# Kernel tuning notes

Hardware: AMD Instinct MI355X
Metric: run time of the kernel (lower is better)

The kernel has to match this reference:

```python
import jax, jax.numpy as jnp
import numpy as np

N_IN, N_OUT, K, G = 128, 256, 3, 3  # G = grid intervals (setup hard-codes 3)
KNOT_LO, KNOT_HI = -1.0, 1.0


def make_grid(n, k, G, lo=KNOT_LO, hi=KNOT_HI):
    # Augmented knot vector: G+1 knots extended by k on each side -> G+2k+1 points
    h = (hi - lo) / G
    g = jnp.arange(-k, G + k + 1, dtype=jnp.float32) * h + lo
    return jnp.tile(g[None, :], (n, 1))  # (n, G+2k+1)


def get_spline_basis(x, grid, k):
    # Cox-de Boor recursion. x: (batch, n); grid: (n, G+2k+1)
    g = grid[None, :, :]          # (1, n, G+2k+1)
    xx = x[:, :, None]            # (batch, n, 1)
    # order-0 (indicator) basis: (batch, n, G+2k)
    basis = ((xx >= g[..., :-1]) & (xx < g[..., 1:])).astype(x.dtype)
    for kk in range(1, k + 1):
        left = (xx - g[..., : -(kk + 1)]) / (g[..., kk:-1] - g[..., : -(kk + 1)]) * basis[..., :-1]
        right = (g[..., kk + 1 :] - xx) / (g[..., kk + 1 :] - g[..., 1:-kk]) * basis[..., 1:]
        basis = left + right
    return basis  # (batch, n, G+k)


def setup_inputs() -> dict:
    key = jax.random.key(0)
    k1, k2 = jax.random.split(key)
    batch = 512
    n = N_IN * N_OUT
    x = jax.random.normal(k1, (batch, N_IN), dtype=jnp.float32)
    grid = make_grid(n, K, G)                                        # state (non-trainable)
    c_basis = 0.1 * jax.random.normal(k2, (n, G + K), dtype=jnp.float32)
    c_spl = jnp.ones((n,), dtype=jnp.float32)
    c_res = jnp.ones((n,), dtype=jnp.float32)
    return {"x": x, "grid": grid, "c_basis": c_basis, "c_spl": c_spl, "c_res": c_res}


def reference(x, grid, c_basis, c_spl, c_res):
    batch = x.shape[0]
    # Broadcast each input node to every output edge, out-major ordering:
    # einsum('ij,k->ikj', x, ones(n_out)).reshape(batch, n_in*n_out)
    x_ext = jnp.broadcast_to(x[:, None, :], (batch, N_OUT, N_IN)).reshape(batch, N_OUT * N_IN)
    # residual branch: swish, transposed to (n, batch)
    res = jax.nn.swish(x_ext).T
    # spline branch: (batch, n, G+K) basis combined with per-edge coeffs -> (n, batch)
    Bi = get_spline_basis(x_ext, grid, K)
    spl = jnp.einsum('ij,bij->ib', c_basis, Bi)
    y = c_spl[:, None] * spl + c_res[:, None] * res            # (n, batch)
    y = y.reshape(N_OUT, N_IN, batch).sum(axis=1) / N_IN       # (n_out, batch)
    return y.T                                                 # (batch, n_out)
```

## Files before the change

kernel.cpp:

```cpp
#include <hip/hip_runtime.h>
#include <hip/hip_bf16.h>


typedef short short8 __attribute__((ext_vector_type(8)));
typedef float f32x4 __attribute__((ext_vector_type(4)));

static __device__ inline unsigned short bf16_bits(float f) {
    union { __hip_bfloat16 h; unsigned short u; } cvt;
    cvt.h = __float2bfloat16(f);
    return cvt.u;
}

__global__ __launch_bounds__(256) void build_fw(
    const float* __restrict__ x,
    const float* __restrict__ grid,
    const float* __restrict__ c_basis,
    const float* __restrict__ c_spl,
    const float* __restrict__ c_res,
    unsigned short* __restrict__ F,
    unsigned short* __restrict__ W)
{
    const int tid = blockIdx.x * 256 + threadIdx.x;

    if (tid < 512 * 128) {
        float t[10];
#pragma unroll
        for (int m = 0; m < 10; ++m) t[m] = grid[m];

        const float xv = x[tid];

        float b0[9];
#pragma unroll
        for (int s = 0; s < 9; ++s)
            b0[s] = (xv >= t[s] && xv < t[s + 1]) ? 1.0f : 0.0f;
        float b1[8];
#pragma unroll
        for (int s = 0; s < 8; ++s)
            b1[s] = (xv - t[s]) / (t[s + 1] - t[s]) * b0[s]
                  + (t[s + 2] - xv) / (t[s + 2] - t[s + 1]) * b0[s + 1];
        float b2[7];
#pragma unroll
        for (int s = 0; s < 7; ++s)
            b2[s] = (xv - t[s]) / (t[s + 2] - t[s]) * b1[s]
                  + (t[s + 3] - xv) / (t[s + 3] - t[s + 1]) * b1[s + 1];
        float b3[6];
#pragma unroll
        for (int s = 0; s < 6; ++s)
            b3[s] = (xv - t[s]) / (t[s + 3] - t[s]) * b2[s]
                  + (t[s + 4] - xv) / (t[s + 4] - t[s + 1]) * b2[s + 1];

        const float sw = xv / (1.0f + expf(-xv));

        unsigned short* dst = F + tid * 7;
#pragma unroll
        for (int s = 0; s < 6; ++s) dst[s] = bf16_bits(b3[s]);
        dst[6] = bf16_bits(sw);
    } else if (tid < 512 * 128 + 32768) {
        const int j = tid - 512 * 128;
        unsigned short* dst = W + j * 7;
        const float spl = c_spl[j];
#pragma unroll
        for (int s = 0; s < 6; ++s) dst[s] = bf16_bits(spl * c_basis[j * 6 + s]);
        dst[6] = bf16_bits(c_res[j]);
    }
}

__global__ __launch_bounds__(64) void kan_gemm(
    const unsigned short* __restrict__ F,
    const unsigned short* __restrict__ W,
    float* __restrict__ out)
{
    const int bt   = blockIdx.x >> 4;
    const int ot   = blockIdx.x & 15;
    const int lane = threadIdx.x;
    const int r    = lane & 15;
    const int q    = lane >> 4;

    const unsigned short* fp = F + (bt * 16 + r) * 896 + q * 8;
    const unsigned short* wp = W + (ot * 16 + r) * 896 + q * 8;

    f32x4 acc = {0.0f, 0.0f, 0.0f, 0.0f};

#pragma unroll
    for (int k0 = 0; k0 < 896; k0 += 128) {
        short8 a0 = *(const short8*)(fp + k0);
        short8 a1 = *(const short8*)(fp + k0 + 32);
        short8 a2 = *(const short8*)(fp + k0 + 64);
        short8 a3 = *(const short8*)(fp + k0 + 96);
        short8 w0 = *(const short8*)(wp + k0);
        short8 w1 = *(const short8*)(wp + k0 + 32);
        short8 w2 = *(const short8*)(wp + k0 + 64);
        short8 w3 = *(const short8*)(wp + k0 + 96);
        acc = __builtin_amdgcn_mfma_f32_16x16x32_bf16(a0, w0, acc, 0, 0, 0);
        acc = __builtin_amdgcn_mfma_f32_16x16x32_bf16(a1, w1, acc, 0, 0, 0);
        acc = __builtin_amdgcn_mfma_f32_16x16x32_bf16(a2, w2, acc, 0, 0, 0);
        acc = __builtin_amdgcn_mfma_f32_16x16x32_bf16(a3, w3, acc, 0, 0, 0);
    }

    const float scale = 1.0f / 128.0f;
    const int orow = bt * 16 + q * 4;
    const int ocol = ot * 16 + r;
#pragma unroll
    for (int reg = 0; reg < 4; ++reg)
        out[(orow + reg) * 256 + ocol] = acc[reg] * scale;
}

extern "C" void kernel_launch(void* const* d_in, const int* in_sizes, int n_in,
                              void* d_out, int out_size, void* d_ws, size_t ws_size,
                              hipStream_t stream) {
    const float* x       = (const float*)d_in[0];
    const float* grid    = (const float*)d_in[1];
    const float* c_basis = (const float*)d_in[2];
    const float* c_spl   = (const float*)d_in[3];
    const float* c_res   = (const float*)d_in[4];
    float* out = (float*)d_out;

    unsigned short* F = (unsigned short*)d_ws;
    unsigned short* W = (unsigned short*)((char*)d_ws + 512 * 896 * 2);

    build_fw<<<384, 256, 0, stream>>>(x, grid, c_basis, c_spl, c_res, F, W);
    kan_gemm<<<512, 64, 0, stream>>>(F, W, out);
}
```

Measured before the change: 68.12 us.

## Fuse spline-basis construction into MFMA GEMM kernel, removing workspace round trip

```diff
diff --git a/kernel.cpp b/kernel.cpp
--- a/kernel.cpp
+++ b/kernel.cpp
@@ -11,63 +11,12 @@
     return cvt.u;
 }
 
-__global__ __launch_bounds__(256) void build_fw(
+__global__ __launch_bounds__(64) void kan_fused(
     const float* __restrict__ x,
     const float* __restrict__ grid,
     const float* __restrict__ c_basis,
     const float* __restrict__ c_spl,
     const float* __restrict__ c_res,
-    unsigned short* __restrict__ F,
-    unsigned short* __restrict__ W)
-{
-    const int tid = blockIdx.x * 256 + threadIdx.x;
-
-    if (tid < 512 * 128) {
-        float t[10];
-#pragma unroll
-        for (int m = 0; m < 10; ++m) t[m] = grid[m];
-
-        const float xv = x[tid];
-
-        float b0[9];
-#pragma unroll
-        for (int s = 0; s < 9; ++s)
-            b0[s] = (xv >= t[s] && xv < t[s + 1]) ? 1.0f : 0.0f;
-        float b1[8];
-#pragma unroll
-        for (int s = 0; s < 8; ++s)
-            b1[s] = (xv - t[s]) / (t[s + 1] - t[s]) * b0[s]
-                  + (t[s + 2] - xv) / (t[s + 2] - t[s + 1]) * b0[s + 1];
-        float b2[7];
-#pragma unroll
-        for (int s = 0; s < 7; ++s)
-            b2[s] = (xv - t[s]) / (t[s + 2] - t[s]) * b1[s]
-                  + (t[s + 3] - xv) / (t[s + 3] - t[s + 1]) * b1[s + 1];
-        float b3[6];
-#pragma unroll
-        for (int s = 0; s < 6; ++s)
-            b3[s] = (xv - t[s]) / (t[s + 3] - t[s]) * b2[s]
-                  + (t[s + 4] - xv) / (t[s + 4] - t[s + 1]) * b2[s + 1];
-
-        const float sw = xv / (1.0f + expf(-xv));
-
-        unsigned short* dst = F + tid * 7;
-#pragma unroll
-        for (int s = 0; s < 6; ++s) dst[s] = bf16_bits(b3[s]);
-        dst[6] = bf16_bits(sw);
-    } else if (tid < 512 * 128 + 32768) {
-        const int j = tid - 512 * 128;
-        unsigned short* dst = W + j * 7;
-        const float spl = c_spl[j];
-#pragma unroll
-        for (int s = 0; s < 6; ++s) dst[s] = bf16_bits(spl * c_basis[j * 6 + s]);
-        dst[6] = bf16_bits(c_res[j]);
-    }
-}
-
-__global__ __launch_bounds__(64) void kan_gemm(
-    const unsigned short* __restrict__ F,
-    const unsigned short* __restrict__ W,
     float* __restrict__ out)
 {
     const int bt   = blockIdx.x >> 4;
@@ -76,30 +25,82 @@
     const int r    = lane & 15;
     const int q    = lane >> 4;
 
-    const unsigned short* fp = F + (bt * 16 + r) * 896 + q * 8;
-    const unsigned short* wp = W + (ot * 16 + r) * 896 + q * 8;
+    const int b = bt * 16 + r;
+    const int o = ot * 16 + r;
+
+    const float t0    = grid[0];
+    const float h     = grid[4] - grid[3];
+    const float inv_h = 1.0f / h;
+
+    const float* xrow = x + b * 128;
+    const int    jb   = o * 128;
 
     f32x4 acc = {0.0f, 0.0f, 0.0f, 0.0f};
 
+#pragma unroll 4
+    for (int c = 0; c < 32; ++c) {
+        const int i = 4 * c + q;
+
+        const float xv = xrow[i];
+        const float u  = (xv - t0) * inv_h;
+
+        float d[10];
 #pragma unroll
-    for (int k0 = 0; k0 < 896; k0 += 128) {
-        short8 a0 = *(const short8*)(fp + k0);
-        short8 a1 = *(const short8*)(fp + k0 + 32);
-        short8 a2 = *(const short8*)(fp + k0 + 64);
-        short8 a3 = *(const short8*)(fp + k0 + 96);
-        short8 w0 = *(const short8*)(wp + k0);
-        short8 w1 = *(const short8*)(wp + k0 + 32);
-        short8 w2 = *(const short8*)(wp + k0 + 64);
-        short8 w3 = *(const short8*)(wp + k0 + 96);
-        acc = __builtin_amdgcn_mfma_f32_16x16x32_bf16(a0, w0, acc, 0, 0, 0);
-        acc = __builtin_amdgcn_mfma_f32_16x16x32_bf16(a1, w1, acc, 0, 0, 0);
-        acc = __builtin_amdgcn_mfma_f32_16x16x32_bf16(a2, w2, acc, 0, 0, 0);
-        acc = __builtin_amdgcn_mfma_f32_16x16x32_bf16(a3, w3, acc, 0, 0, 0);
+        for (int s = 0; s < 10; ++s) d[s] = u - (float)s;
+
+        float I0[9];
+#pragma unroll
+        for (int s = 0; s < 9; ++s)
+            I0[s] = (d[s] >= 0.0f && d[s + 1] < 0.0f) ? 1.0f : 0.0f;
+
+        float b1[8];
+#pragma unroll
+        for (int s = 0; s < 8; ++s)
+            b1[s] = d[s] * I0[s] - d[s + 2] * I0[s + 1];
+
+        float b2[7];
+#pragma unroll
+        for (int s = 0; s < 7; ++s)
+            b2[s] = d[s] * b1[s] - d[s + 3] * b1[s + 1];
+
+        float b3[6];
+#pragma unroll
+        for (int s = 0; s < 6; ++s)
+            b3[s] = (d[s] * b2[s] - d[s + 4] * b2[s + 1]) * (1.0f / 6.0f);
+
+        const float e  = __expf(-xv);
+        const float sw = xv * __builtin_amdgcn_rcpf(1.0f + e);
+
+        short8 af;
+        af[0] = bf16_bits(b3[0]);
+        af[1] = bf16_bits(b3[1]);
+        af[2] = bf16_bits(b3[2]);
+        af[3] = bf16_bits(b3[3]);
+        af[4] = bf16_bits(b3[4]);
+        af[5] = bf16_bits(b3[5]);
+        af[6] = bf16_bits(sw);
+        af[7] = 0;
+
+        const int    j   = jb + i;
+        const float* cbp = c_basis + j * 6;
+        const float  spl = c_spl[j];
+
+        short8 bfr;
+        bfr[0] = bf16_bits(spl * cbp[0]);
+        bfr[1] = bf16_bits(spl * cbp[1]);
+        bfr[2] = bf16_bits(spl * cbp[2]);
+        bfr[3] = bf16_bits(spl * cbp[3]);
+        bfr[4] = bf16_bits(spl * cbp[4]);
+        bfr[5] = bf16_bits(spl * cbp[5]);
+        bfr[6] = bf16_bits(c_res[j]);
+        bfr[7] = 0;
+
+        acc = __builtin_amdgcn_mfma_f32_16x16x32_bf16(af, bfr, acc, 0, 0, 0);
     }
 
     const float scale = 1.0f / 128.0f;
-    const int orow = bt * 16 + q * 4;
-    const int ocol = ot * 16 + r;
+    const int   orow  = bt * 16 + q * 4;
+    const int   ocol  = ot * 16 + r;
 #pragma unroll
     for (int reg = 0; reg < 4; ++reg)
         out[(orow + reg) * 256 + ocol] = acc[reg] * scale;
@@ -115,9 +116,5 @@
     const float* c_res   = (const float*)d_in[4];
     float* out = (float*)d_out;
 
-    unsigned short* F = (unsigned short*)d_ws;
-    unsigned short* W = (unsigned short*)((char*)d_ws + 512 * 896 * 2);
-
-    build_fw<<<384, 256, 0, stream>>>(x, grid, c_basis, c_spl, c_res, F, W);
-    kan_gemm<<<512, 64, 0, stream>>>(F, W, out);
+    kan_fused<<<512, 64, 0, stream>>>(x, grid, c_basis, c_spl, c_res, out);
 }
```

Measured after the change: 86.30 us. +26.7%, slower.

## Pad feature rows to 8 bf16 with vector stores and closed-form uniform B-splines

Applied to the files above, without the earlier changes.

```diff
diff --git a/kernel.cpp b/kernel.cpp
--- a/kernel.cpp
+++ b/kernel.cpp
@@ -23,45 +23,64 @@
     const int tid = blockIdx.x * 256 + threadIdx.x;
 
     if (tid < 512 * 128) {
-        float t[10];
-#pragma unroll
-        for (int m = 0; m < 10; ++m) t[m] = grid[m];
+        const float t0    = grid[0];
+        const float inv_h = 1.0f / (grid[1] - grid[0]);
 
         const float xv = x[tid];
+        const float u  = (xv - t0) * inv_h;
 
-        float b0[9];
+        float d[10];
+#pragma unroll
+        for (int s = 0; s < 10; ++s) d[s] = u - (float)s;
+
+        float I0[9];
 #pragma unroll
         for (int s = 0; s < 9; ++s)
-            b0[s] = (xv >= t[s] && xv < t[s + 1]) ? 1.0f : 0.0f;
+            I0[s] = (d[s] >= 0.0f && d[s + 1] < 0.0f) ? 1.0f : 0.0f;
+
         float b1[8];
 #pragma unroll
         for (int s = 0; s < 8; ++s)
-            b1[s] = (xv - t[s]) / (t[s + 1] - t[s]) * b0[s]
-                  + (t[s + 2] - xv) / (t[s + 2] - t[s + 1]) * b0[s + 1];
+            b1[s] = d[s] * I0[s] - d[s + 2] * I0[s + 1];
+
         float b2[7];
 #pragma unroll
         for (int s = 0; s < 7; ++s)
-            b2[s] = (xv - t[s]) / (t[s + 2] - t[s]) * b1[s]
-                  + (t[s + 3] - xv) / (t[s + 3] - t[s + 1]) * b1[s + 1];
+            b2[s] = d[s] * b1[s] - d[s + 3] * b1[s + 1];
+
         float b3[6];
 #pragma unroll
         for (int s = 0; s < 6; ++s)
-            b3[s] = (xv - t[s]) / (t[s + 3] - t[s]) * b2[s]
-                  + (t[s + 4] - xv) / (t[s + 4] - t[s + 1]) * b2[s + 1];
+            b3[s] = (d[s] * b2[s] - d[s + 4] * b2[s + 1]) * (1.0f / 6.0f);
 
-        const float sw = xv / (1.0f + expf(-xv));
+        const float e  = __expf(-xv);
+        const float sw = xv * __builtin_amdgcn_rcpf(1.0f + e);
 
-        unsigned short* dst = F + tid * 7;
-#pragma unroll
-        for (int s = 0; s < 6; ++s) dst[s] = bf16_bits(b3[s]);
-        dst[6] = bf16_bits(sw);
+        short8 v;
+        v[0] = bf16_bits(b3[0]);
+        v[1] = bf16_bits(b3[1]);
+        v[2] = bf16_bits(b3[2]);
+        v[3] = bf16_bits(b3[3]);
+        v[4] = bf16_bits(b3[4]);
+        v[5] = bf16_bits(b3[5]);
+        v[6] = bf16_bits(sw);
+        v[7] = 0;
+        *(short8*)(F + tid * 8) = v;
     } else if (tid < 512 * 128 + 32768) {
         const int j = tid - 512 * 128;
-        unsigned short* dst = W + j * 7;
         const float spl = c_spl[j];
-#pragma unroll
-        for (int s = 0; s < 6; ++s) dst[s] = bf16_bits(spl * c_basis[j * 6 + s]);
-        dst[6] = bf16_bits(c_res[j]);
+        const float* cbp = c_basis + j * 6;
+
+        short8 v;
+        v[0] = bf16_bits(spl * cbp[0]);
+        v[1] = bf16_bits(spl * cbp[1]);
+        v[2] = bf16_bits(spl * cbp[2]);
+        v[3] = bf16_bits(spl * cbp[3]);
+        v[4] = bf16_bits(spl * cbp[4]);
+        v[5] = bf16_bits(spl * cbp[5]);
+        v[6] = bf16_bits(c_res[j]);
+        v[7] = 0;
+        *(short8*)(W + j * 8) = v;
     }
 }
 
@@ -76,13 +95,13 @@
     const int r    = lane & 15;
     const int q    = lane >> 4;
 
-    const unsigned short* fp = F + (bt * 16 + r) * 896 + q * 8;
-    const unsigned short* wp = W + (ot * 16 + r) * 896 + q * 8;
+    const unsigned short* fp = F + (bt * 16 + r) * 1024 + q * 8;
+    const unsigned short* wp = W + (ot * 16 + r) * 1024 + q * 8;
 
     f32x4 acc = {0.0f, 0.0f, 0.0f, 0.0f};
 
 #pragma unroll
-    for (int k0 = 0; k0 < 896; k0 += 128) {
+    for (int k0 = 0; k0 < 1024; k0 += 128) {
         short8 a0 = *(const short8*)(fp + k0);
         short8 a1 = *(const short8*)(fp + k0 + 32);
         short8 a2 = *(const short8*)(fp + k0 + 64);
@@ -98,8 +117,8 @@
     }
 
     const float scale = 1.0f / 128.0f;
-    const int orow = bt * 16 + q * 4;
-    const int ocol = ot * 16 + r;
+    const int   orow  = bt * 16 + q * 4;
+    const int   ocol  = ot * 16 + r;
 #pragma unroll
     for (int reg = 0; reg < 4; ++reg)
         out[(orow + reg) * 256 + ocol] = acc[reg] * scale;
@@ -116,7 +135,7 @@
     float* out = (float*)d_out;
 
     unsigned short* F = (unsigned short*)d_ws;
-    unsigned short* W = (unsigned short*)((char*)d_ws + 512 * 896 * 2);
+    unsigned short* W = (unsigned short*)((char*)d_ws + 512 * 1024 * 2);
 
     build_fw<<<384, 256, 0, stream>>>(x, grid, c_basis, c_spl, c_res, F, W);
     kan_gemm<<<512, 64, 0, stream>>>(F, W, out);
```

Measured after the change: 67.65 us. About the same (-0.7%).
